# Optimization experiments

Measured on AMD Instinct MI355X. Metric: run time of the kernel, lower is better.

The kernel has to match this reference:

```python
import jax, jax.numpy as jnp
import numpy as np

CHARS_SIZE = 10000
HIDDEN = 1024
OUTPUT = 100
BATCH = 4096
MAXLEN = 2048


def setup_inputs() -> dict:
    key = jax.random.key(0)
    k1, k2, k3 = jax.random.split(key, 3)
    words_t = jax.random.randint(k1, (BATCH, MAXLEN), 0, CHARS_SIZE, dtype=jnp.int64 if jax.config.jax_enable_x64 else jnp.int32)
    # Xavier-uniform init like the torch module
    lim1 = float(np.sqrt(6.0 / (CHARS_SIZE + HIDDEN)))
    lim2 = float(np.sqrt(6.0 / (HIDDEN + OUTPUT)))
    W1 = jax.random.uniform(k2, (HIDDEN, CHARS_SIZE), jnp.float32, -lim1, lim1)
    b1 = jnp.zeros((HIDDEN,), jnp.float32)
    W2 = jax.random.uniform(k3, (OUTPUT, HIDDEN), jnp.float32, -lim2, lim2)
    b2 = jnp.zeros((OUTPUT,), jnp.float32)
    return {"words_t": words_t, "W1": W1, "b1": b1, "W2": W2, "b2": b2}


def reference(words_t, W1, b1, W2, b2):
    batch, maxlen = words_t.shape
    # Direct scatter-add histogram: equivalent to one-hot(batch,maxlen,chars)
    # summed over maxlen, without materializing the dense one-hot tensor.
    hist = jnp.zeros((batch, CHARS_SIZE), jnp.float32)
    rows = jnp.arange(batch)[:, None]  # (batch, 1) broadcast over maxlen
    hist = hist.at[rows, words_t].add(1.0)
    hid = hist @ W1.T + b1            # (batch, hidden)
    out = hid @ W2.T + b2             # (batch, output)
    return out
```

## Files before the change

kernel.cpp:

```cpp
#include <hip/hip_runtime.h>
#include <stdint.h>

#define CHARS   10000
#define KPAD    10240
#define HIDDEN  1024
#define OUTPUT  100
#define OPAD    128
#define BATCH   4096
#define MAXLEN  2048

typedef __bf16 bf16_t;
typedef __bf16 bf16x8 __attribute__((ext_vector_type(8)));
typedef __bf16 bf16x4 __attribute__((ext_vector_type(4)));
typedef float  f32x4  __attribute__((ext_vector_type(4)));
typedef uint32_t u32x4 __attribute__((ext_vector_type(4)));

__device__ __forceinline__ void gload16(const bf16_t* g, bf16_t* l) {
    __builtin_amdgcn_global_load_lds(
        (__attribute__((address_space(1))) void*)const_cast<bf16_t*>(g),
        (__attribute__((address_space(3))) void*)l, 16, 0, 0);
}

__global__ void k_prep(const float* __restrict__ W1, bf16_t* __restrict__ W1b,
                       const float* __restrict__ W2, float* __restrict__ W2T,
                       const float* __restrict__ b1, float* __restrict__ hid) {
    const int bid = blockIdx.x, tid = threadIdx.x;
    if (bid < 2048) {
        const int N4 = (KPAD / 4) * HIDDEN;
        for (int i = bid * 256 + tid; i < N4; i += 2048 * 256) {
            int c4 = i % (KPAD / 4);
            int h  = i / (KPAD / 4);
            bf16x4 o;
            if (c4 * 4 < CHARS) {
                f32x4 v = *(const f32x4*)(W1 + (size_t)h * CHARS + (size_t)c4 * 4);
                o[0] = (bf16_t)v[0]; o[1] = (bf16_t)v[1];
                o[2] = (bf16_t)v[2]; o[3] = (bf16_t)v[3];
            } else {
                o[0] = o[1] = o[2] = o[3] = (bf16_t)0.0f;
            }
            *(bf16x4*)(W1b + (size_t)h * KPAD + (size_t)c4 * 4) = o;
        }
    } else if (bid < 2560) {
        int i = (bid - 2048) * 256 + tid;
        int o = i & (OPAD - 1), k = i >> 7;
        W2T[i] = (o < OUTPUT) ? W2[(size_t)o * HIDDEN + k] : 0.0f;
    } else {
        const int M4 = BATCH * HIDDEN / 4;
        for (int i = (bid - 2560) * 256 + tid; i < M4; i += 2048 * 256) {
            int h4 = i & (HIDDEN / 4 - 1);
            ((f32x4*)hid)[i] = ((const f32x4*)b1)[h4];
        }
    }
}

__device__ __forceinline__ void hist_body(uint32_t* h, const int* __restrict__ words,
                                          bf16_t* __restrict__ hist, int row,
                                          int dstRow, int tid) {
#pragma unroll
    for (int i = 0; i < KPAD / 4 / 256; ++i)
        *(u32x4*)(h + (i * 256 + tid) * 4) = (u32x4){0u, 0u, 0u, 0u};
    __syncthreads();
    const int* w = words + (size_t)row * MAXLEN;
#pragma unroll
    for (int i = 0; i < MAXLEN / 4 / 256; ++i) {
        int4 t4 = *(const int4*)(w + (i * 256 + tid) * 4);
        atomicAdd(&h[t4.x], 1u); atomicAdd(&h[t4.y], 1u);
        atomicAdd(&h[t4.z], 1u); atomicAdd(&h[t4.w], 1u);
    }
    __syncthreads();
    bf16_t* dst = hist + (size_t)dstRow * KPAD;
#pragma unroll
    for (int i = 0; i < KPAD / 8 / 256; ++i) {
        int j = (i * 256 + tid) * 8;
        bf16x8 o;
#pragma unroll
        for (int q = 0; q < 8; ++q) o[q] = (bf16_t)(float)h[j + q];
        *(bf16x8*)(dst + j) = o;
    }
}

__global__ void k_hist(const int* __restrict__ words, bf16_t* __restrict__ hist,
                       int rowStart) {
    __shared__ uint32_t h[KPAD];
    hist_body(h, words, hist, rowStart + blockIdx.x, blockIdx.x, threadIdx.x);
}

__global__ void k_preph(const int* __restrict__ words, bf16_t* __restrict__ hist,
                        const float* __restrict__ W1, bf16_t* __restrict__ W1b,
                        const float* __restrict__ W2, float* __restrict__ W2T,
                        const float* __restrict__ b1, float* __restrict__ hid,
                        int initHid) {
    __shared__ uint32_t h[KPAD];
    const int bid = blockIdx.x, tid = threadIdx.x;
    if (bid < BATCH) {
        hist_body(h, words, hist, bid, bid, tid);
    } else if (bid < BATCH + 2048) {
        const int b2i = bid - BATCH;
        const int N4 = (KPAD / 4) * HIDDEN;
        for (int i = b2i * 256 + tid; i < N4; i += 2048 * 256) {
            int c4 = i % (KPAD / 4);
            int hh = i / (KPAD / 4);
            bf16x4 o;
            if (c4 * 4 < CHARS) {
                f32x4 v = *(const f32x4*)(W1 + (size_t)hh * CHARS + (size_t)c4 * 4);
                o[0] = (bf16_t)v[0]; o[1] = (bf16_t)v[1];
                o[2] = (bf16_t)v[2]; o[3] = (bf16_t)v[3];
            } else {
                o[0] = o[1] = o[2] = o[3] = (bf16_t)0.0f;
            }
            *(bf16x4*)(W1b + (size_t)hh * KPAD + (size_t)c4 * 4) = o;
        }
    } else if (bid < BATCH + 2560) {
        int i = (bid - BATCH - 2048) * 256 + tid;
        int o = i & (OPAD - 1), k = i >> 7;
        W2T[i] = (o < OUTPUT) ? W2[(size_t)o * HIDDEN + k] : 0.0f;
    } else if (initHid) {
        const int b2i = bid - BATCH - 2560;
        const int M4 = BATCH * HIDDEN / 4;
        for (int i = b2i * 256 + tid; i < M4; i += 2048 * 256) {
            int h4 = i & (HIDDEN / 4 - 1);
            ((f32x4*)hid)[i] = ((const f32x4*)b1)[h4];
        }
    }
}

template <int EPI>
__global__ void __launch_bounds__(512)
k_gemm(const bf16_t* __restrict__ A, const bf16_t* __restrict__ Bt,
       float* __restrict__ hid, float* __restrict__ extraSlabs,
       int KT, int mtiles) {
    __shared__ __attribute__((aligned(16))) bf16_t As[2][2][128 * 64];
    __shared__ __attribute__((aligned(16))) bf16_t Bs[2][2][128 * 64];

    const int nblk = gridDim.x;
    int idx = blockIdx.x;
    if ((nblk & 7) == 0) idx = (idx & 7) * (nblk >> 3) + (idx >> 3);
    const int mt = idx % mtiles;
    const int ns = idx / mtiles;
    const int m0 = mt * 256;
    const int n0 = (ns & 3) * 256;
    const int kbeg = (ns >> 2) * KT;

    const int tid  = threadIdx.x;
    const int lane = tid & 63;
    const int wave = tid >> 6;
    const int wm64 = (wave >> 2) * 64;
    const int wn32 = (wave & 3) * 32;
    const int l15  = lane & 15;
    const int hi   = lane >> 4;
    const int x3   = l15 & 7;

    int arow[4], brow[2], koff[2];
#pragma unroll
    for (int fi = 0; fi < 4; ++fi) arow[fi] = (wm64 + fi * 16 + l15) * 128;
#pragma unroll
    for (int fj = 0; fj < 2; ++fj) brow[fj] = (wn32 + fj * 16 + l15) * 128;
#pragma unroll
    for (int kk = 0; kk < 2; ++kk) koff[kk] = ((((kk << 2) | hi)) ^ x3) * 16;

    const int srow = lane >> 3;
    const int csw8 = ((lane & 7) ^ srow) * 8;
    const bf16_t* Ab = A  + (size_t)(m0 + wave * 16 + srow) * KPAD + csw8;
    const bf16_t* Bb = Bt + (size_t)(n0 + wave * 16 + srow) * KPAD + csw8;
    const int wsl = wave * 2 * 512;

    f32x4 acc[2][2][4][2] = {};
    bf16x8 Afa0[2][4], Afa1[2][4], Bfa0[2][4], Bfa1[2][4];
    bf16x8 Afb0[2][2], Afb1[2][2], Bfb0[2][2], Bfb1[2][2];

#define STAGE(SB, SOP, SH, KTILE_) do {                                        \
    int kte_ = (KTILE_); if (kte_ >= KT) kte_ = 0;             \
    const size_t kc_ = (size_t)(kbeg + kte_) * 64;                             \
    const bf16_t* gb_ = (SOP) ? Bb : Ab;                                       \
    bf16_t* lb_ = ((SOP) ? &Bs[SB][SH][0] : &As[SB][SH][0]) + wsl;             \
    gload16(gb_ + (size_t)((SH) * 128)     * KPAD + kc_, lb_);                 \
    gload16(gb_ + (size_t)((SH) * 128 + 8) * KPAD + kc_, lb_ + 512);           \
} while (0)

#define LOADA(DST, PB, HALF) do {                                              \
    const char* p_ = (const char*)&As[PB][HALF][0];                            \
    _Pragma("unroll") for (int kk = 0; kk < 2; ++kk)                           \
        _Pragma("unroll") for (int fi = 0; fi < 4; ++fi)                       \
            DST[kk][fi] = *(const bf16x8*)(p_ + arow[fi] + koff[kk]);          \
} while (0)

#define LOADB(DST, PB, HALF) do {                                              \
    const char* p_ = (const char*)&Bs[PB][HALF][0];                            \
    _Pragma("unroll") for (int kk = 0; kk < 2; ++kk)                           \
        _Pragma("unroll") for (int fj = 0; fj < 2; ++fj)                       \
            DST[kk][fj] = *(const bf16x8*)(p_ + brow[fj] + koff[kk]);          \
} while (0)

#define PHB() do {                                                             \
    __builtin_amdgcn_sched_barrier(0);                                         \
    __builtin_amdgcn_s_barrier();                                              \
    __builtin_amdgcn_sched_barrier(0);                                         \
} while (0)

#define VM4() asm volatile("s_waitcnt vmcnt(4)" ::: "memory")

#define MMQ(QI, QJ, FA, FB) do {                                               \
    __builtin_amdgcn_s_setprio(1);                                             \
    _Pragma("unroll") for (int kk = 0; kk < 2; ++kk)                           \
        _Pragma("unroll") for (int fi = 0; fi < 4; ++fi)                       \
            _Pragma("unroll") for (int fj = 0; fj < 2; ++fj)                   \
                acc[QI][QJ][fi][fj] = __builtin_amdgcn_mfma_f32_16x16x32_bf16( \
                    FA[kk][fi], FB[kk][fj], acc[QI][QJ][fi][fj], 0, 0, 0);     \
    __builtin_amdgcn_s_setprio(0);                                             \
} while (0)

    STAGE(0, 0, 0, 0);
    STAGE(0, 1, 0, 0);
    STAGE(0, 0, 1, 0);
    STAGE(0, 1, 1, 0);
    STAGE(1, 1, 0, 1);
    STAGE(1, 0, 0, 1);
    VM4();
    PHB();
    LOADA(Afa0, 0, 0);
    LOADB(Afb0, 0, 0);

    for (int kt = 0; kt < KT; kt += 2) {
        PHB();
        STAGE(1, 0, 1, kt + 1);
        LOADA(Afa1, 0, 1);
        MMQ(0, 0, Afa0, Afb0);
        VM4();
        PHB();
        STAGE(1, 1, 1, kt + 1);
        LOADB(Afb1, 0, 1);
        MMQ(1, 0, Afa1, Afb0);
        PHB();
        STAGE(0, 1, 0, kt + 2);
        MMQ(0, 1, Afa0, Afb1);
        VM4();
        PHB();
        STAGE(0, 0, 0, kt + 2);
        LOADA(Bfa0, 1, 0);
        LOADB(Bfb0, 1, 0);
        MMQ(1, 1, Afa1, Afb1);
        PHB();
        STAGE(0, 0, 1, kt + 2);
        LOADA(Bfa1, 1, 1);
        MMQ(0, 0, Bfa0, Bfb0);
        VM4();
        PHB();
        STAGE(0, 1, 1, kt + 2);
        LOADB(Bfb1, 1, 1);
        MMQ(1, 0, Bfa1, Bfb0);
        PHB();
        STAGE(1, 1, 0, kt + 3);
        MMQ(0, 1, Bfa0, Bfb1);
        VM4();
        PHB();
        STAGE(1, 0, 0, kt + 3);
        LOADA(Afa0, 0, 0);
        LOADB(Afb0, 0, 0);
        MMQ(1, 1, Bfa1, Bfb1);
    }
#undef MMQ
#undef VM4
#undef PHB
#undef LOADB
#undef LOADA
#undef STAGE

    const int er = hi * 4;
    float* dstBase;
    if (EPI == 1) {
        const int s = ns >> 2;
        dstBase = (s == 0) ? hid : extraSlabs + (size_t)(s - 1) * BATCH * HIDDEN;
    } else {
        dstBase = hid;
    }
#pragma unroll
    for (int qi = 0; qi < 2; ++qi)
#pragma unroll
    for (int qj = 0; qj < 2; ++qj)
#pragma unroll
    for (int fi = 0; fi < 4; ++fi)
#pragma unroll
    for (int fj = 0; fj < 2; ++fj) {
        float* dst = dstBase + (size_t)(m0 + qi * 128 + wm64 + fi * 16 + er) * HIDDEN
                             + (n0 + qj * 128 + wn32 + fj * 16 + l15);
#pragma unroll
        for (int r = 0; r < 4; ++r) {
            if (EPI == 1) dst[(size_t)r * HIDDEN] = acc[qi][qj][fi][fj][r];
            else          atomicAdd(dst + (size_t)r * HIDDEN, acc[qi][qj][fi][fj][r]);
        }
    }
}

__global__ void k_red(float* __restrict__ hid, const float* __restrict__ extra,
                      const float* __restrict__ b1) {
    const int N4 = BATCH * HIDDEN / 4;
    const float* e0 = extra;
    const float* e1 = extra + (size_t)BATCH * HIDDEN;
    const float* e2 = extra + (size_t)2 * BATCH * HIDDEN;
    for (int i = blockIdx.x * 256 + threadIdx.x; i < N4; i += 2048 * 256) {
        int h4 = i & (HIDDEN / 4 - 1);
        f32x4 v = ((const f32x4*)hid)[i];
        v += ((const f32x4*)b1)[h4];
        v += ((const f32x4*)e0)[i];
        v += ((const f32x4*)e1)[i];
        v += ((const f32x4*)e2)[i];
        ((f32x4*)hid)[i] = v;
    }
}

__global__ void k_out(const float* __restrict__ hid, const float* __restrict__ W2T,
                      const float* __restrict__ b2, float* __restrict__ out) {
    const int tid = threadIdx.x;
    const int o4  = (tid & 31) * 4;
    const int rs  = tid >> 5;
    const int row = blockIdx.x * 8 + rs;
    const float* hrow = hid + (size_t)row * HIDDEN;
    f32x4 acc = {0.f, 0.f, 0.f, 0.f};
    for (int k0 = 0; k0 < HIDDEN; k0 += 4) {
        f32x4 hv = *(const f32x4*)(hrow + k0);
#pragma unroll
        for (int q = 0; q < 4; ++q) {
            f32x4 wv = *(const f32x4*)(W2T + (size_t)(k0 + q) * OPAD + o4);
            acc += hv[q] * wv;
        }
    }
    if (o4 < OUTPUT) {
        float* op = out + (size_t)row * OUTPUT + o4;
#pragma unroll
        for (int q = 0; q < 4; ++q)
            op[q] = acc[q] + b2[o4 + q];
    }
}

static inline int pick_S(int mtiles) {
    const int cands[10] = {80, 40, 20, 16, 10, 8, 5, 4, 2, 1};
    for (int i = 0; i < 10; ++i)
        if (mtiles * 4 * cands[i] <= 256) return cands[i];
    return 1;
}

extern "C" void kernel_launch(void* const* d_in, const int* in_sizes, int n_in,
                              void* d_out, int out_size, void* d_ws, size_t ws_size,
                              hipStream_t stream) {
    (void)in_sizes; (void)n_in; (void)out_size;
    const int*   words = (const int*)d_in[0];
    const float* W1    = (const float*)d_in[1];
    const float* b1    = (const float*)d_in[2];
    const float* W2    = (const float*)d_in[3];
    const float* b2    = (const float*)d_in[4];
    float* out = (float*)d_out;

    char* ws = (char*)d_ws;
    size_t off = 0;
    bf16_t* W1b  = (bf16_t*)(ws + off); off += (size_t)HIDDEN * KPAD * sizeof(bf16_t);
    float*  hid  = (float*) (ws + off); off += (size_t)BATCH * HIDDEN * sizeof(float);
    float*  W2T  = (float*) (ws + off); off += (size_t)HIDDEN * OPAD * sizeof(float);
    const size_t slabBytes = (size_t)BATCH * HIDDEN * sizeof(float);
    const size_t histBytes = (size_t)BATCH * KPAD * sizeof(bf16_t);

    if (ws_size >= off + 3 * slabBytes + histBytes) {
        float* extra = (float*)(ws + off);
        bf16_t* histC = (bf16_t*)(ws + off + 3 * slabBytes);
        k_preph<<<dim3(BATCH + 4608), dim3(256), 0, stream>>>(
            words, histC, W1, W1b, W2, W2T, b1, hid, 0);
        int mtiles = BATCH / 256;
        int S = 4;
        int KT = (KPAD / 64) / S;
        k_gemm<1><<<dim3(mtiles * 4 * S), dim3(512), 0, stream>>>(
            histC, W1b, hid, extra, KT, mtiles);
        k_red<<<dim3(2048), dim3(256), 0, stream>>>(hid, extra, b1);
    } else {
        bf16_t* histC = (bf16_t*)(ws + off);
        size_t rem = (ws_size > off) ? (ws_size - off) : 0;
        int chunkRows = (int)(rem / ((size_t)KPAD * sizeof(bf16_t)));
        chunkRows = (chunkRows / 256) * 256;
        if (chunkRows > BATCH) chunkRows = BATCH;
        if (chunkRows < 256)   chunkRows = 256;

        if (chunkRows >= BATCH) {
            k_preph<<<dim3(BATCH + 4608), dim3(256), 0, stream>>>(
                words, histC, W1, W1b, W2, W2T, b1, hid, 1);
            int mtiles = BATCH / 256;
            int S = pick_S(mtiles);
            int KT = (KPAD / 64) / S;
            k_gemm<0><<<dim3(mtiles * 4 * S), dim3(512), 0, stream>>>(
                histC, W1b, hid, nullptr, KT, mtiles);
        } else {
            k_prep<<<dim3(4608), dim3(256), 0, stream>>>(W1, W1b, W2, W2T, b1, hid);
            for (int r0 = 0; r0 < BATCH; r0 += chunkRows) {
                int rows = BATCH - r0;
                if (rows > chunkRows) rows = chunkRows;
                k_hist<<<dim3(rows), dim3(256), 0, stream>>>(words, histC, r0);
                int mtiles = rows / 256;
                int S = pick_S(mtiles);
                int KT = (KPAD / 64) / S;
                k_gemm<0><<<dim3(mtiles * 4 * S), dim3(512), 0, stream>>>(
                    histC, W1b, hid + (size_t)r0 * HIDDEN, nullptr, KT, mtiles);
            }
        }
    }

    k_out<<<dim3(BATCH / 8), dim3(256), 0, stream>>>(hid, W2T, b2, out);
}
```

Before: 297.7 us.

## Rework GEMM mainloop into triple-buffered BK=32 pipeline with one barrier per tile

Replaces the hand-scheduled double-buffered 64-wide K pipeline, which split each tile into halves and used many phase barriers, with a three-stage rotating LDS buffer of 32-wide K tiles. Each iteration issues the global-to-LDS loads two tiles ahead, runs 32 MFMAs from the current buffer, and then waits and synchronises once. The swizzle is adapted to the narrower rows. It also drops the setprio hints and the interleaving of LDS reads with MFMAs, which may expose more latency. Halving the K tile doubles the iteration count and the barrier overhead per unit of work.

```diff
diff --git a/kernel.cpp b/kernel.cpp
--- a/kernel.cpp
+++ b/kernel.cpp
@@ -8,6 +8,7 @@
 #define OPAD    128
 #define BATCH   4096
 #define MAXLEN  2048
+#define BK      32
 
 typedef __bf16 bf16_t;
 typedef __bf16 bf16x8 __attribute__((ext_vector_type(8)));
@@ -129,8 +130,8 @@
 k_gemm(const bf16_t* __restrict__ A, const bf16_t* __restrict__ Bt,
        float* __restrict__ hid, float* __restrict__ extraSlabs,
        int KT, int mtiles) {
-    __shared__ __attribute__((aligned(16))) bf16_t As[2][2][128 * 64];
-    __shared__ __attribute__((aligned(16))) bf16_t Bs[2][2][128 * 64];
+    __shared__ __attribute__((aligned(16))) bf16_t As[3][256 * BK];
+    __shared__ __attribute__((aligned(16))) bf16_t Bs[3][256 * BK];
 
     const int nblk = gridDim.x;
     int idx = blockIdx.x;
@@ -148,122 +149,86 @@
     const int wn32 = (wave & 3) * 32;
     const int l15  = lane & 15;
     const int hi   = lane >> 4;
-    const int x3   = l15 & 7;
-
-    int arow[4], brow[2], koff[2];
-#pragma unroll
-    for (int fi = 0; fi < 4; ++fi) arow[fi] = (wm64 + fi * 16 + l15) * 128;
-#pragma unroll
-    for (int fj = 0; fj < 2; ++fj) brow[fj] = (wn32 + fj * 16 + l15) * 128;
-#pragma unroll
-    for (int kk = 0; kk < 2; ++kk) koff[kk] = ((((kk << 2) | hi)) ^ x3) * 16;
-
-    const int srow = lane >> 3;
-    const int csw8 = ((lane & 7) ^ srow) * 8;
+    const int x2   = l15 & 3;
+    const int koff = ((hi ^ x2)) * 16;
+
+    int arow[4], brow[2];
+#pragma unroll
+    for (int fi = 0; fi < 4; ++fi) arow[fi] = (wm64 + fi * 16 + l15) * (BK * 2);
+#pragma unroll
+    for (int fj = 0; fj < 2; ++fj) brow[fj] = (wn32 + fj * 16 + l15) * (BK * 2);
+
+    const int srow = lane >> 2;
+    const int csw8 = ((lane & 3) ^ (srow & 3)) * 8;
     const bf16_t* Ab = A  + (size_t)(m0 + wave * 16 + srow) * KPAD + csw8;
     const bf16_t* Bb = Bt + (size_t)(n0 + wave * 16 + srow) * KPAD + csw8;
-    const int wsl = wave * 2 * 512;
+    const int wso = wave * 512;
 
     f32x4 acc[2][2][4][2] = {};
-    bf16x8 Afa0[2][4], Afa1[2][4], Bfa0[2][4], Bfa1[2][4];
-    bf16x8 Afb0[2][2], Afb1[2][2], Bfb0[2][2], Bfb1[2][2];
-
-#define STAGE(SB, SOP, SH, KTILE_) do {                                        \
+
+#define STAGE4(DA, DB, KTILE_) do {                                            \
     int kte_ = (KTILE_); if (kte_ >= KT) kte_ = 0;             \
-    const size_t kc_ = (size_t)(kbeg + kte_) * 64;                             \
-    const bf16_t* gb_ = (SOP) ? Bb : Ab;                                       \
-    bf16_t* lb_ = ((SOP) ? &Bs[SB][SH][0] : &As[SB][SH][0]) + wsl;             \
-    gload16(gb_ + (size_t)((SH) * 128)     * KPAD + kc_, lb_);                 \
-    gload16(gb_ + (size_t)((SH) * 128 + 8) * KPAD + kc_, lb_ + 512);           \
-} while (0)
-
-#define LOADA(DST, PB, HALF) do {                                              \
-    const char* p_ = (const char*)&As[PB][HALF][0];                            \
-    _Pragma("unroll") for (int kk = 0; kk < 2; ++kk)                           \
-        _Pragma("unroll") for (int fi = 0; fi < 4; ++fi)                       \
-            DST[kk][fi] = *(const bf16x8*)(p_ + arow[fi] + koff[kk]);          \
-} while (0)
-
-#define LOADB(DST, PB, HALF) do {                                              \
-    const char* p_ = (const char*)&Bs[PB][HALF][0];                            \
-    _Pragma("unroll") for (int kk = 0; kk < 2; ++kk)                           \
-        _Pragma("unroll") for (int fj = 0; fj < 2; ++fj)                       \
-            DST[kk][fj] = *(const bf16x8*)(p_ + brow[fj] + koff[kk]);          \
-} while (0)
-
-#define PHB() do {                                                             \
-    __builtin_amdgcn_sched_barrier(0);                                         \
-    __builtin_amdgcn_s_barrier();                                              \
-    __builtin_amdgcn_sched_barrier(0);                                         \
-} while (0)
-
-#define VM4() asm volatile("s_waitcnt vmcnt(4)" ::: "memory")
-
-#define MMQ(QI, QJ, FA, FB) do {                                               \
-    __builtin_amdgcn_s_setprio(1);                                             \
-    _Pragma("unroll") for (int kk = 0; kk < 2; ++kk)                           \
-        _Pragma("unroll") for (int fi = 0; fi < 4; ++fi)                       \
-            _Pragma("unroll") for (int fj = 0; fj < 2; ++fj)                   \
-                acc[QI][QJ][fi][fj] = __builtin_amdgcn_mfma_f32_16x16x32_bf16( \
-                    FA[kk][fi], FB[kk][fj], acc[QI][QJ][fi][fj], 0, 0, 0);     \
-    __builtin_amdgcn_s_setprio(0);                                             \
-} while (0)
-
-    STAGE(0, 0, 0, 0);
-    STAGE(0, 1, 0, 0);
-    STAGE(0, 0, 1, 0);
-    STAGE(0, 1, 1, 0);
-    STAGE(1, 1, 0, 1);
-    STAGE(1, 0, 0, 1);
-    VM4();
-    PHB();
-    LOADA(Afa0, 0, 0);
-    LOADB(Afb0, 0, 0);
-
-    for (int kt = 0; kt < KT; kt += 2) {
-        PHB();
-        STAGE(1, 0, 1, kt + 1);
-        LOADA(Afa1, 0, 1);
-        MMQ(0, 0, Afa0, Afb0);
-        VM4();
-        PHB();
-        STAGE(1, 1, 1, kt + 1);
-        LOADB(Afb1, 0, 1);
-        MMQ(1, 0, Afa1, Afb0);
-        PHB();
-        STAGE(0, 1, 0, kt + 2);
-        MMQ(0, 1, Afa0, Afb1);
-        VM4();
-        PHB();
-        STAGE(0, 0, 0, kt + 2);
-        LOADA(Bfa0, 1, 0);
-        LOADB(Bfb0, 1, 0);
-        MMQ(1, 1, Afa1, Afb1);
-        PHB();
-        STAGE(0, 0, 1, kt + 2);
-        LOADA(Bfa1, 1, 1);
-        MMQ(0, 0, Bfa0, Bfb0);
-        VM4();
-        PHB();
-        STAGE(0, 1, 1, kt + 2);
-        LOADB(Bfb1, 1, 1);
-        MMQ(1, 0, Bfa1, Bfb0);
-        PHB();
-        STAGE(1, 1, 0, kt + 3);
-        MMQ(0, 1, Bfa0, Bfb1);
-        VM4();
-        PHB();
-        STAGE(1, 0, 0, kt + 3);
-        LOADA(Afa0, 0, 0);
-        LOADB(Afb0, 0, 0);
-        MMQ(1, 1, Bfa1, Bfb1);
-    }
-#undef MMQ
-#undef VM4
-#undef PHB
-#undef LOADB
-#undef LOADA
-#undef STAGE
+    const size_t kc_ = (size_t)(kbeg + kte_) * BK;                             \
+    gload16(Ab + kc_,                        (DA) + wso);                      \
+    gload16(Ab + (size_t)128 * KPAD + kc_,   (DA) + 4096 + wso);               \
+    gload16(Bb + kc_,                        (DB) + wso);                      \
+    gload16(Bb + (size_t)128 * KPAD + kc_,   (DB) + 4096 + wso);               \
+} while (0)
+
+#define LDA4(DST, BASE, QOFF) do {                                            \
+    _Pragma("unroll") for (int fi = 0; fi < 4; ++fi)                          \
+        DST[fi] = *(const bf16x8*)((const char*)(BASE) + (QOFF) +             \
+                                   arow[fi] + koff);                          \
+} while (0)
+
+#define LDB2(DST, BASE, QOFF) do {                                            \
+    _Pragma("unroll") for (int fj = 0; fj < 2; ++fj)                          \
+        DST[fj] = *(const bf16x8*)((const char*)(BASE) + (QOFF) +             \
+                                   brow[fj] + koff);                          \
+} while (0)
+
+#define MM8(QI, QJ, FA, FB) do {                                              \
+    _Pragma("unroll") for (int fi = 0; fi < 4; ++fi)                          \
+        _Pragma("unroll") for (int fj = 0; fj < 2; ++fj)                      \
+            acc[QI][QJ][fi][fj] = __builtin_amdgcn_mfma_f32_16x16x32_bf16(    \
+                FA[fi], FB[fj], acc[QI][QJ][fi][fj], 0, 0, 0);                \
+} while (0)
+
+#define TILEBAR() do {                                                        \
+    asm volatile("s_waitcnt vmcnt(4)" ::: "memory");                          \
+    __builtin_amdgcn_sched_barrier(0);                                        \
+    __builtin_amdgcn_s_barrier();                                             \
+    __builtin_amdgcn_sched_barrier(0);                                        \
+} while (0)
+
+    bf16_t *rdA = &As[0][0], *nxA = &As[1][0], *stA = &As[2][0];
+    bf16_t *rdB = &Bs[0][0], *nxB = &Bs[1][0], *stB = &Bs[2][0];
+
+    STAGE4(rdA, rdB, 0);
+    STAGE4(nxA, nxB, 1);
+    TILEBAR();
+
+    for (int t = 0; t < KT; ++t) {
+        STAGE4(stA, stB, t + 2);
+        bf16x8 fa[4], ga[4], fb[2], gb[2];
+        LDA4(fa, rdA, 0);
+        LDB2(fb, rdB, 0);
+        MM8(0, 0, fa, fb);
+        LDA4(ga, rdA, 8192);
+        MM8(1, 0, ga, fb);
+        LDB2(gb, rdB, 8192);
+        MM8(0, 1, fa, gb);
+        MM8(1, 1, ga, gb);
+        TILEBAR();
+        bf16_t* tp;
+        tp = rdA; rdA = nxA; nxA = stA; stA = tp;
+        tp = rdB; rdB = nxB; nxB = stB; stB = tp;
+    }
+#undef TILEBAR
+#undef MM8
+#undef LDB2
+#undef LDA4
+#undef STAGE4
 
     const int er = hi * 4;
     float* dstBase;
@@ -365,7 +330,7 @@
             words, histC, W1, W1b, W2, W2T, b1, hid, 0);
         int mtiles = BATCH / 256;
         int S = 4;
-        int KT = (KPAD / 64) / S;
+        int KT = (KPAD / BK) / S;
         k_gemm<1><<<dim3(mtiles * 4 * S), dim3(512), 0, stream>>>(
             histC, W1b, hid, extra, KT, mtiles);
         k_red<<<dim3(2048), dim3(256), 0, stream>>>(hid, extra, b1);
@@ -382,7 +347,7 @@
                 words, histC, W1, W1b, W2, W2T, b1, hid, 1);
             int mtiles = BATCH / 256;
             int S = pick_S(mtiles);
-            int KT = (KPAD / 64) / S;
+            int KT = (KPAD / BK) / S;
             k_gemm<0><<<dim3(mtiles * 4 * S), dim3(512), 0, stream>>>(
                 histC, W1b, hid, nullptr, KT, mtiles);
         } else {
@@ -393,7 +358,7 @@
                 k_hist<<<dim3(rows), dim3(256), 0, stream>>>(words, histC, r0);
                 int mtiles = rows / 256;
                 int S = pick_S(mtiles);
-                int KT = (KPAD / 64) / S;
+                int KT = (KPAD / BK) / S;
                 k_gemm<0><<<dim3(mtiles * 4 * S), dim3(512), 0, stream>>>(
                     histC, W1b, hid + (size_t)r0 * HIDDEN, nullptr, KT, mtiles);
             }
```

Measured after the change: 318.4 us. 6.9% more time.

## Fuse split-K reduction into output GEMV and simplify W1 conversion indexing

Applied to the files above, without the earlier changes.

Removes the separate reduction kernel that summed the four split-K slabs plus bias into hid. The final output kernel now reads the slabs directly, adds b1 on the fly, and splits K across four warps per row with a shared-memory reduction. This avoids writing hid back and reading it again. The W1 bf16 conversion also now maps two blocks per hidden row with a fixed loop, which removes the div/mod indexing.

```diff
diff --git a/kernel.cpp b/kernel.cpp
--- a/kernel.cpp
+++ b/kernel.cpp
@@ -26,19 +26,19 @@
                        const float* __restrict__ b1, float* __restrict__ hid) {
     const int bid = blockIdx.x, tid = threadIdx.x;
     if (bid < 2048) {
-        const int N4 = (KPAD / 4) * HIDDEN;
-        for (int i = bid * 256 + tid; i < N4; i += 2048 * 256) {
-            int c4 = i % (KPAD / 4);
-            int h  = i / (KPAD / 4);
+        const int row = bid >> 1;
+        const int g0  = (bid & 1) * 1280;
+        for (int j = 0; j < 5; ++j) {
+            int c4 = g0 + j * 256 + tid;
             bf16x4 o;
             if (c4 * 4 < CHARS) {
-                f32x4 v = *(const f32x4*)(W1 + (size_t)h * CHARS + (size_t)c4 * 4);
+                f32x4 v = *(const f32x4*)(W1 + (size_t)row * CHARS + (size_t)c4 * 4);
                 o[0] = (bf16_t)v[0]; o[1] = (bf16_t)v[1];
                 o[2] = (bf16_t)v[2]; o[3] = (bf16_t)v[3];
             } else {
                 o[0] = o[1] = o[2] = o[3] = (bf16_t)0.0f;
             }
-            *(bf16x4*)(W1b + (size_t)h * KPAD + (size_t)c4 * 4) = o;
+            *(bf16x4*)(W1b + (size_t)row * KPAD + (size_t)c4 * 4) = o;
         }
     } else if (bid < 2560) {
         int i = (bid - 2048) * 256 + tid;
@@ -96,19 +96,19 @@
         hist_body(h, words, hist, bid, bid, tid);
     } else if (bid < BATCH + 2048) {
         const int b2i = bid - BATCH;
-        const int N4 = (KPAD / 4) * HIDDEN;
-        for (int i = b2i * 256 + tid; i < N4; i += 2048 * 256) {
-            int c4 = i % (KPAD / 4);
-            int hh = i / (KPAD / 4);
+        const int row = b2i >> 1;
+        const int g0  = (b2i & 1) * 1280;
+        for (int j = 0; j < 5; ++j) {
+            int c4 = g0 + j * 256 + tid;
             bf16x4 o;
             if (c4 * 4 < CHARS) {
-                f32x4 v = *(const f32x4*)(W1 + (size_t)hh * CHARS + (size_t)c4 * 4);
+                f32x4 v = *(const f32x4*)(W1 + (size_t)row * CHARS + (size_t)c4 * 4);
                 o[0] = (bf16_t)v[0]; o[1] = (bf16_t)v[1];
                 o[2] = (bf16_t)v[2]; o[3] = (bf16_t)v[3];
             } else {
                 o[0] = o[1] = o[2] = o[3] = (bf16_t)0.0f;
             }
-            *(bf16x4*)(W1b + (size_t)hh * KPAD + (size_t)c4 * 4) = o;
+            *(bf16x4*)(W1b + (size_t)row * KPAD + (size_t)c4 * 4) = o;
         }
     } else if (bid < BATCH + 2560) {
         int i = (bid - BATCH - 2048) * 256 + tid;
@@ -291,20 +291,45 @@
     }
 }
 
-__global__ void k_red(float* __restrict__ hid, const float* __restrict__ extra,
-                      const float* __restrict__ b1) {
-    const int N4 = BATCH * HIDDEN / 4;
-    const float* e0 = extra;
-    const float* e1 = extra + (size_t)BATCH * HIDDEN;
-    const float* e2 = extra + (size_t)2 * BATCH * HIDDEN;
-    for (int i = blockIdx.x * 256 + threadIdx.x; i < N4; i += 2048 * 256) {
-        int h4 = i & (HIDDEN / 4 - 1);
-        f32x4 v = ((const f32x4*)hid)[i];
-        v += ((const f32x4*)b1)[h4];
-        v += ((const f32x4*)e0)[i];
-        v += ((const f32x4*)e1)[i];
-        v += ((const f32x4*)e2)[i];
-        ((f32x4*)hid)[i] = v;
+__global__ void k_outf(const float* __restrict__ hid, const float* __restrict__ extra,
+                       const float* __restrict__ W2T, const float* __restrict__ b1,
+                       const float* __restrict__ b2, float* __restrict__ out) {
+    __shared__ float red[8][128];
+    const int tid  = threadIdx.x;
+    const int o4   = (tid & 31) * 4;
+    const int slot = tid >> 5;
+    const int row  = blockIdx.x * 2 + (slot >> 2);
+    const int kc   = slot & 3;
+    const float* h0 = hid + (size_t)row * HIDDEN;
+    const float* e0 = extra + (size_t)row * HIDDEN;
+    const float* e1 = e0 + (size_t)BATCH * HIDDEN;
+    const float* e2 = e1 + (size_t)BATCH * HIDDEN;
+    f32x4 acc = {0.f, 0.f, 0.f, 0.f};
+    const int k0beg = kc * 256;
+#pragma unroll 4
+    for (int k0 = k0beg; k0 < k0beg + 256; k0 += 4) {
+        f32x4 hv = *(const f32x4*)(h0 + k0);
+        hv += *(const f32x4*)(b1 + k0);
+        hv += *(const f32x4*)(e0 + k0);
+        hv += *(const f32x4*)(e1 + k0);
+        hv += *(const f32x4*)(e2 + k0);
+#pragma unroll
+        for (int q = 0; q < 4; ++q) {
+            f32x4 wv = *(const f32x4*)(W2T + (size_t)(k0 + q) * OPAD + o4);
+            acc += hv[q] * wv;
+        }
+    }
+    *(f32x4*)&red[slot][o4] = acc;
+    __syncthreads();
+    if (kc == 0 && o4 < OUTPUT) {
+        f32x4 r = *(const f32x4*)&red[slot][o4];
+        r += *(const f32x4*)&red[slot + 1][o4];
+        r += *(const f32x4*)&red[slot + 2][o4];
+        r += *(const f32x4*)&red[slot + 3][o4];
+        float* op = out + (size_t)row * OUTPUT + o4;
+#pragma unroll
+        for (int q = 0; q < 4; ++q)
+            op[q] = r[q] + b2[o4 + q];
     }
 }
 
@@ -368,7 +393,8 @@
         int KT = (KPAD / 64) / S;
         k_gemm<1><<<dim3(mtiles * 4 * S), dim3(512), 0, stream>>>(
             histC, W1b, hid, extra, KT, mtiles);
-        k_red<<<dim3(2048), dim3(256), 0, stream>>>(hid, extra, b1);
+        k_outf<<<dim3(BATCH / 2), dim3(256), 0, stream>>>(
+            hid, extra, W2T, b1, b2, out);
     } else {
         bf16_t* histC = (bf16_t*)(ws + off);
         size_t rem = (ws_size > off) ? (ws_size - off) : 0;
@@ -398,7 +424,6 @@
                     histC, W1b, hid + (size_t)r0 * HIDDEN, nullptr, KT, mtiles);
             }
         }
-    }
-
-    k_out<<<dim3(BATCH / 8), dim3(256), 0, stream>>>(hid, W2T, b2, out);
-}
+        k_out<<<dim3(BATCH / 8), dim3(256), 0, stream>>>(hid, W2T, b2, out);
+    }
+}
```

After: 353.8 us. +18.8%, slower.
